# Kernel tuning notes

Hardware: AMD Instinct MI355X
Metric: run time of the kernel (lower is better)

Reference implementation:

```python
import jax, jax.numpy as jnp
import numpy as np

VOCAB, EMB = 30000, 300
HEADS, DPH = 8, 50
AD = HEADS * DPH            # att_dim_total = 400
MAX_LINES, MAX_WPL = 128, 32
BATCH = 16
NEG = 1e7                   # padding-mask penalty, matches torch source


def _split_heads(x):
    # [N, S, AD] -> [N, H, S, D]
    return x.reshape(x.shape[0], -1, HEADS, DPH).transpose(0, 2, 1, 3)


def _attention(q, k, v, mask_q=None, mask_k=None, mask_v=None):
    # Faithful port of MTHiSAN._attention. Note the (oddly named) torch masks:
    #   mask_q masks the KEY axis of scores, mask_k/mask_v zero the QUERY axis.
    scale = float(np.sqrt(q.shape[-1]))
    scores = jnp.einsum('bhqd,bhkd->bhqk', q, k) / scale
    if mask_q is not None:
        scores = scores - NEG * (~mask_q)[:, None, None, :].astype(scores.dtype)
    w = jax.nn.softmax(scores, axis=-1)
    if mask_k is not None:
        w = w * mask_k[:, None, :, None].astype(w.dtype)
    out = jnp.einsum('bhqk,bhkd->bhqd', w, v)
    if mask_v is not None:
        out = out * mask_v[:, None, :, None].astype(out.dtype)
    return out


def _forward(docs, emb, wq_w, wq_b, wk_w, wk_b, wv_w, wv_b, w_tgt,
             lq_w, lq_b, lk_w, lk_b, lv_w, lv_b, l_tgt,
             fc1_w, fc1_b, fc2_w, fc2_b):
    B = docs.shape[0]
    d = docs[:, :MAX_LINES * MAX_WPL].reshape(B * MAX_LINES, MAX_WPL)
    mask_w = d != 0                               # [B*L, W]
    mask_l = mask_w.sum(-1) != 0                  # [B*L]  non-empty lines
    # NOTE: instead of gathering non-empty lines (data-dependent shape), we keep
    # full shapes; masked word attention yields exact zeros for empty lines,
    # equivalent to the torch scatter into new_zeros.
    we = emb[d]                                   # [B*L, W, E] (dropout = eval/no-op)
    wq = jax.nn.elu(_split_heads(we @ wq_w + wq_b))
    wk = jax.nn.elu(_split_heads(we @ wk_w + wk_b))
    wv = jax.nn.elu(_split_heads(we @ wv_w + wv_b))
    watt = _attention(wq, wk, wv, mask_w, mask_w, mask_w)   # [B*L,H,W,D]
    # learned word-level target query (Linear(1, AD)(ones) == weight vector)
    tgt = jnp.broadcast_to(w_tgt.reshape(1, HEADS, 1, DPH),
                           (B * MAX_LINES, HEADS, 1, DPH))
    line_e = _attention(tgt, wk, watt, mask_q=mask_w)       # [B*L,H,1,D]
    line_e = line_e.transpose(0, 2, 1, 3).reshape(B * MAX_LINES, AD)
    line_e = line_e * mask_l[:, None].astype(line_e.dtype)  # zero empty lines
    line_e = line_e.reshape(B, MAX_LINES, AD)
    mask_l2 = mask_l.reshape(B, MAX_LINES)
    lq = jax.nn.elu(_split_heads(line_e @ lq_w + lq_b))
    lk = jax.nn.elu(_split_heads(line_e @ lk_w + lk_b))
    lv = jax.nn.elu(_split_heads(line_e @ lv_w + lv_b))
    latt = _attention(lq, lk, lv, mask_l2, mask_l2, mask_l2)  # [B,H,L,D]
    dtgt = jnp.broadcast_to(l_tgt.reshape(1, HEADS, 1, DPH), (B, HEADS, 1, DPH))
    doc_e = _attention(dtgt, lk, latt, mask_q=mask_l2)        # [B,H,1,D]
    doc_e = doc_e.transpose(0, 2, 1, 3).reshape(B, AD)
    logits1 = doc_e @ fc1_w + fc1_b   # task 'site'      [B,70]
    logits2 = doc_e @ fc2_w + fc2_b   # task 'histology' [B,512]
    return jnp.concatenate([logits1, logits2], axis=1)


def setup_inputs() -> dict:
    key = jax.random.key(0)
    ks = jax.random.split(key, 20)
    xavier = lambda k, i, o: (jax.random.normal(k, (i, o), jnp.float32)
                              * np.float32(np.sqrt(2.0 / (i + o))))
    emb = jax.random.normal(ks[0], (VOCAB, EMB), jnp.float32) * 0.02
    emb = emb.at[0].set(0.0)  # padding row zeroed as in __init__
    docs = jax.random.randint(ks[1], (BATCH, MAX_LINES * MAX_WPL), 0, VOCAB)
    z = lambda n: jnp.zeros((n,), jnp.float32)
    return dict(
        docs=docs, emb=emb,
        wq_w=xavier(ks[2], EMB, AD), wq_b=z(AD),
        wk_w=xavier(ks[3], EMB, AD), wk_b=z(AD),
        wv_w=xavier(ks[4], EMB, AD), wv_b=z(AD),
        w_tgt=jax.random.uniform(ks[5], (AD,), jnp.float32),
        lq_w=xavier(ks[6], AD, AD), lq_b=z(AD),
        lk_w=xavier(ks[7], AD, AD), lk_b=z(AD),
        lv_w=xavier(ks[8], AD, AD), lv_b=z(AD),
        l_tgt=jax.random.uniform(ks[9], (AD,), jnp.float32),
        fc1_w=xavier(ks[10], AD, 70), fc1_b=z(70),
        fc2_w=xavier(ks[11], AD, 512), fc2_b=z(512),
    )


def reference(docs, emb, wq_w, wq_b, wk_w, wk_b, wv_w, wv_b, w_tgt,
              lq_w, lq_b, lk_w, lk_b, lv_w, lv_b, l_tgt,
              fc1_w, fc1_b, fc2_w, fc2_b):
    return _forward(docs, emb, wq_w, wq_b, wk_w, wk_b, wv_w, wv_b, w_tgt,
                    lq_w, lq_b, lk_w, lk_b, lv_w, lv_b, l_tgt,
                    fc1_w, fc1_b, fc2_w, fc2_b)
```

## Files before the change

kernel.cpp:

```cpp
#include <hip/hip_runtime.h>
#include <math.h>

#define NLINES 2048
#define WPL 32
#define EMBD 300
#define AD 400
#define NH 8
#define DPH 50
#define QKV_S 52
#define SC_S 36
#define BATCH 16
#define LPD 128
#define NCOLS 1200
#define NPAD 1280
#define WLINE_FL 39936
#define HBLK 4992

typedef __bf16 bf16;
typedef bf16  v8bf  __attribute__((ext_vector_type(8)));
typedef float v4f   __attribute__((ext_vector_type(4)));
typedef float v16f  __attribute__((ext_vector_type(16)));

__device__ __forceinline__ float elu(float x) {
    return x > 0.f ? x : expm1f(x);
}
__device__ __forceinline__ float elu_fast(float x) {
    return x > 0.f ? x : (__expf(x) - 1.f);
}

#define SCALE 7.0710678118654755f

__global__ void split_rows(const float* __restrict__ src,
                           bf16* __restrict__ hi, bf16* __restrict__ lo,
                           int rows, int K, int K2)
{
    long idx = (long)blockIdx.x * 256 + threadIdx.x;
    if (idx >= (long)rows * K2) return;
    int r = (int)(idx / K2), k = (int)(idx - (long)r * K2);
    float x = (k < K) ? src[(long)r * K + k] : 0.f;
    bf16 h = (bf16)x;
    float hf = (float)h;
    bf16 l = (bf16)(x - hf);
    hi[idx] = h; lo[idx] = l;
}

__global__ void split_wt(const float* __restrict__ W0, const float* __restrict__ W1,
                         const float* __restrict__ W2,
                         const float* __restrict__ B0, const float* __restrict__ B1,
                         const float* __restrict__ B2,
                         bf16* __restrict__ hi, bf16* __restrict__ lo,
                         float* __restrict__ biasCat, int K, int K2)
{
    long idx = (long)blockIdx.x * 256 + threadIdx.x;
    if (idx >= (long)NPAD * K2) return;
    int n = (int)(idx / K2), k = (int)(idx - (long)n * K2);
    float x = 0.f;
    if (k < K && n < NCOLS) {
        int p = n / 400, c = n - p * 400;
        const float* W = (p == 0) ? W0 : (p == 1) ? W1 : W2;
        x = W[(long)k * 400 + c];
    }
    bf16 h = (bf16)x;
    float hf = (float)h;
    bf16 l = (bf16)(x - hf);
    hi[idx] = h; lo[idx] = l;
    if (k == 0) {
        float b = 0.f;
        if (n < NCOLS) {
            int p = n / 400, c = n - p * 400;
            const float* Bp = (p == 0) ? B0 : (p == 1) ? B1 : B2;
            b = Bp[c];
        }
        biasCat[n] = b;
    }
}

__launch_bounds__(256)
__global__ void mfma_gemm(const bf16* __restrict__ Ah_t, const bf16* __restrict__ Al_t,
                          const int* __restrict__ docs,
                          const bf16* __restrict__ Bh_t, const bf16* __restrict__ Bl_t,
                          const float* __restrict__ biasCat,
                          float* __restrict__ C, int K2, int word_layout)
{
    __shared__ __align__(16) bf16 Ah[4096];
    __shared__ __align__(16) bf16 Al[4096];
    __shared__ __align__(16) bf16 Bh[4096];
    __shared__ __align__(16) bf16 Bl[4096];
    __shared__ int tok[128];

    const int tid = threadIdx.x;
    const int row0 = blockIdx.y * 128;
    const int n0 = blockIdx.x * 128;

    if (tid < 128) tok[tid] = docs ? docs[row0 + tid] : (row0 + tid);
    __syncthreads();

    const int qa = tid >> 7;
    const int sm = tid & 127;
    const long aoff = (long)tok[sm] * K2;
    const long boff = (long)(n0 + sm) * K2;

    const int wv = tid >> 6, lane = tid & 63;
    const int half = lane >> 5, r32 = lane & 31;
    const int wm0 = (wv >> 1) * 64, wn0 = (wv & 1) * 64;

    v16f acc[2][2];
    #pragma unroll
    for (int a = 0; a < 2; ++a)
        #pragma unroll
        for (int b = 0; b < 2; ++b) acc[a][b] = (v16f)0.f;

    const int nk = K2 >> 5;
    v8bf pa0 = *(const v8bf*)(Ah_t + aoff + qa * 8);
    v8bf pa1 = *(const v8bf*)(Ah_t + aoff + (qa + 2) * 8);
    v8bf pl0 = *(const v8bf*)(Al_t + aoff + qa * 8);
    v8bf pl1 = *(const v8bf*)(Al_t + aoff + (qa + 2) * 8);
    v8bf pb0 = *(const v8bf*)(Bh_t + boff + qa * 8);
    v8bf pb1 = *(const v8bf*)(Bh_t + boff + (qa + 2) * 8);
    v8bf pc0 = *(const v8bf*)(Bl_t + boff + qa * 8);
    v8bf pc1 = *(const v8bf*)(Bl_t + boff + (qa + 2) * 8);

    for (int kt = 0; kt < nk; ++kt) {
        *(v8bf*)&Ah[tid * 8]         = pa0;
        *(v8bf*)&Ah[(256 + tid) * 8] = pa1;
        *(v8bf*)&Al[tid * 8]         = pl0;
        *(v8bf*)&Al[(256 + tid) * 8] = pl1;
        *(v8bf*)&Bh[tid * 8]         = pb0;
        *(v8bf*)&Bh[(256 + tid) * 8] = pb1;
        *(v8bf*)&Bl[tid * 8]         = pc0;
        *(v8bf*)&Bl[(256 + tid) * 8] = pc1;
        __syncthreads();

        if (kt + 1 < nk) {
            const int k1 = (kt + 1) * 32;
            pa0 = *(const v8bf*)(Ah_t + aoff + k1 + qa * 8);
            pa1 = *(const v8bf*)(Ah_t + aoff + k1 + (qa + 2) * 8);
            pl0 = *(const v8bf*)(Al_t + aoff + k1 + qa * 8);
            pl1 = *(const v8bf*)(Al_t + aoff + k1 + (qa + 2) * 8);
            pb0 = *(const v8bf*)(Bh_t + boff + k1 + qa * 8);
            pb1 = *(const v8bf*)(Bh_t + boff + k1 + (qa + 2) * 8);
            pc0 = *(const v8bf*)(Bl_t + boff + k1 + qa * 8);
            pc1 = *(const v8bf*)(Bl_t + boff + k1 + (qa + 2) * 8);
        }

        v8bf fa_h[2][2], fa_l[2][2], fb_h[2][2], fb_l[2][2];
        #pragma unroll
        for (int t = 0; t < 2; ++t)
            #pragma unroll
            for (int ks = 0; ks < 2; ++ks) {
                const int ea = (((ks * 2 + half) << 7) + wm0 + t * 32 + r32) * 8;
                fa_h[t][ks] = *(const v8bf*)&Ah[ea];
                fa_l[t][ks] = *(const v8bf*)&Al[ea];
                const int eb = (((ks * 2 + half) << 7) + wn0 + t * 32 + r32) * 8;
                fb_h[t][ks] = *(const v8bf*)&Bh[eb];
                fb_l[t][ks] = *(const v8bf*)&Bl[eb];
            }

        #pragma unroll
        for (int ks = 0; ks < 2; ++ks)
            #pragma unroll
            for (int mt = 0; mt < 2; ++mt)
                #pragma unroll
                for (int nt = 0; nt < 2; ++nt)
                    acc[mt][nt] = __builtin_amdgcn_mfma_f32_32x32x16_bf16(fa_h[mt][ks], fb_h[nt][ks], acc[mt][nt], 0, 0, 0);
        #pragma unroll
        for (int ks = 0; ks < 2; ++ks)
            #pragma unroll
            for (int mt = 0; mt < 2; ++mt)
                #pragma unroll
                for (int nt = 0; nt < 2; ++nt)
                    acc[mt][nt] = __builtin_amdgcn_mfma_f32_32x32x16_bf16(fa_h[mt][ks], fb_l[nt][ks], acc[mt][nt], 0, 0, 0);
        #pragma unroll
        for (int ks = 0; ks < 2; ++ks)
            #pragma unroll
            for (int mt = 0; mt < 2; ++mt)
                #pragma unroll
                for (int nt = 0; nt < 2; ++nt)
                    acc[mt][nt] = __builtin_amdgcn_mfma_f32_32x32x16_bf16(fa_l[mt][ks], fb_h[nt][ks], acc[mt][nt], 0, 0, 0);
        __syncthreads();
    }

    if (word_layout) {
        #pragma unroll
        for (int nt = 0; nt < 2; ++nt) {
            const int col = n0 + wn0 + nt * 32 + r32;
            if (col >= NCOLS) continue;
            const float bv = biasCat[col];
            const int p = col / 400;
            const int rem = col - p * 400;
            const int hh = rem / 50;
            const int d  = rem - hh * 50;
            #pragma unroll
            for (int mt = 0; mt < 2; ++mt) {
                const int rbase = row0 + wm0 + mt * 32 + 4 * half;
                #pragma unroll
                for (int rg = 0; rg < 16; ++rg) {
                    const int row = rbase + (rg & 3) + 8 * (rg >> 2);
                    const int ln = row >> 5, r = row & 31;
                    const float x = acc[mt][nt][rg] + bv;
                    C[(((long)ln * NH + hh) * 3 + p) * 1664 + r * 52 + d] = elu_fast(x);
                }
            }
        }
    } else {
        #pragma unroll
        for (int nt = 0; nt < 2; ++nt) {
            const int col = n0 + wn0 + nt * 32 + r32;
            if (col >= NCOLS) continue;
            const float bv = biasCat[col];
            #pragma unroll
            for (int mt = 0; mt < 2; ++mt) {
                const int rbase = row0 + wm0 + mt * 32 + 4 * half;
                #pragma unroll
                for (int rg = 0; rg < 16; ++rg) {
                    const int row = rbase + (rg & 3) + 8 * (rg >> 2);
                    const float x = acc[mt][nt][rg] + bv;
                    C[(long)row * NCOLS + col] = elu_fast(x);
                }
            }
        }
    }
}

__launch_bounds__(256)
__global__ void word_attn4(const float* __restrict__ qkvw, const int* __restrict__ docs,
                           const float* __restrict__ w_tgt,
                           float* __restrict__ line_e, float* __restrict__ mask_l)
{
    __shared__ __align__(16) float sh[HBLK];
    __shared__ float sc[32 * 33];
    __shared__ float msk[WPL];
    __shared__ float tw[WPL];
    __shared__ float coefA[WPL];
    __shared__ float part[8][33];
    __shared__ float cw[WPL];
    __shared__ float vpart[4][64];
    __shared__ float tg[52];
    __shared__ float mls_s;

    const int tid = threadIdx.x;
    const int line = blockIdx.x >> 3;
    const int h = blockIdx.x & 7;

    if (tid < WPL) msk[tid] = (docs[line * WPL + tid] != 0) ? 1.f : 0.f;
    if (tid >= 64 && tid < 116) tg[tid - 64] = (tid - 64 < DPH) ? w_tgt[h * DPH + tid - 64] : 0.f;

    const float* src = qkvw + ((long)line * NH + h) * HBLK;
    for (int i = tid; i < HBLK / 4; i += 256)
        *(float4*)&sh[i * 4] = *(const float4*)&src[i * 4];
    if (tid < 192) {
        const int a = tid / 64, rem = tid - a * 64;
        sh[a * 1664 + (rem >> 1) * 52 + 50 + (rem & 1)] = 0.f;
    }
    __syncthreads();

    if (tid == 0) {
        float m = 0.f;
        for (int w = 0; w < WPL; ++w) m = fmaxf(m, msk[w]);
        mls_s = m;
        if (h == 0) mask_l[line] = m;
    }

    const int j = tid >> 3, kg = tid & 7;
    float4 qv[13];
    #pragma unroll
    for (int i = 0; i < 13; ++i) qv[i] = *(const float4*)&sh[j * 52 + i * 4];

    float e4[4];
    float m = -1e30f;
    #pragma unroll
    for (int c = 0; c < 4; ++c) {
        const int kk = kg * 4 + c;
        const float* kr = &sh[1664 + kk * 52];
        float s = 0.f;
        #pragma unroll
        for (int i = 0; i < 13; ++i) {
            const float4 kv = *(const float4*)&kr[i * 4];
            s += qv[i].x * kv.x + qv[i].y * kv.y + qv[i].z * kv.z + qv[i].w * kv.w;
        }
        s = s / SCALE - 1e7f * (1.f - msk[kk]);
        e4[c] = s;
        m = fmaxf(m, s);
    }
    m = fmaxf(m, __shfl_xor(m, 1));
    m = fmaxf(m, __shfl_xor(m, 2));
    m = fmaxf(m, __shfl_xor(m, 4));
    float rsum = 0.f;
    #pragma unroll
    for (int c = 0; c < 4; ++c) { e4[c] = __expf(e4[c] - m); rsum += e4[c]; }
    rsum += __shfl_xor(rsum, 1);
    rsum += __shfl_xor(rsum, 2);
    rsum += __shfl_xor(rsum, 4);
    #pragma unroll
    for (int c = 0; c < 4; ++c) sc[j * 33 + kg * 4 + c] = e4[c];

    if (tid < WPL) {
        const float* kr = &sh[1664 + tid * 52];
        float s = 0.f;
        #pragma unroll
        for (int i = 0; i < 25; ++i)
            s += tg[2 * i] * kr[2 * i] + tg[2 * i + 1] * kr[2 * i + 1];
        s = s / SCALE - 1e7f * (1.f - msk[tid]);
        float tm = s;
        #pragma unroll
        for (int off = 16; off >= 1; off >>= 1) tm = fmaxf(tm, __shfl_xor(tm, off, 32));
        const float te = __expf(s - tm);
        float tsum = te;
        #pragma unroll
        for (int off = 16; off >= 1; off >>= 1) tsum += __shfl_xor(tsum, off, 32);
        tw[tid] = te / tsum;
    }
    __syncthreads();

    if (kg == 0) coefA[j] = tw[j] * msk[j] / rsum;
    __syncthreads();

    {
        const int k = tid & 31, jg = tid >> 5;
        float cv = 0.f;
        #pragma unroll
        for (int t = 0; t < 4; ++t) {
            const int jj = jg * 4 + t;
            cv += coefA[jj] * sc[jj * 33 + k];
        }
        part[jg][k] = cv;
    }
    __syncthreads();
    if (tid < WPL) {
        float cv = 0.f;
        #pragma unroll
        for (int g = 0; g < 8; ++g) cv += part[g][tid];
        cw[tid] = cv;
    }
    __syncthreads();

    {
        const int d = tid & 63, kh = tid >> 6;
        float acc = 0.f;
        if (d < 52) {
            #pragma unroll
            for (int t = 0; t < 8; ++t) {
                const int k = kh * 8 + t;
                acc += cw[k] * sh[3328 + k * 52 + d];
            }
        }
        vpart[kh][d] = acc;
    }
    __syncthreads();
    if (tid < DPH) {
        const float o = vpart[0][tid] + vpart[1][tid] + vpart[2][tid] + vpart[3][tid];
        line_e[(long)line * AD + h * DPH + tid] = o * mls_s;
    }
}

__launch_bounds__(256)
__global__ void line_attn2(const float* __restrict__ Q, const float* __restrict__ Kp,
                           const float* __restrict__ Vp,
                           long DS, long HS, long LS,
                           const float* __restrict__ l_tgt, const float* __restrict__ mask_l,
                           float* __restrict__ doc_e)
{
    __shared__ float kl[LPD * 52];
    __shared__ float sc[64 * 130];
    __shared__ float ml[LPD];
    __shared__ float tw[LPD];
    __shared__ float cw[LPD];
    __shared__ float coefA[64];
    __shared__ float pm[4 * 64];
    __shared__ float ps[4 * 64];
    __shared__ float tg[52];
    __shared__ float rr[2];
    __shared__ float vpart[2][64];

    const int tid = threadIdx.x;
    const int doc = blockIdx.x >> 3;
    const int h = blockIdx.x & 7;
    const float* qbase = Q + doc * DS + h * HS;
    const float* kbase = Kp + doc * DS + h * HS;
    const float* vbase = Vp + doc * DS + h * HS;

    if (tid < LPD) { ml[tid] = mask_l[doc * LPD + tid]; cw[tid] = 0.f; }
    if (tid < 52) tg[tid] = (tid < DPH) ? l_tgt[h * DPH + tid] : 0.f;
    for (int idx = tid; idx < LPD * 52; idx += 256) {
        const int r = idx / 52, d = idx - r * 52;
        kl[idx] = (d < DPH) ? kbase[(long)r * LS + d] : 0.f;
    }
    __syncthreads();

    if (tid < LPD) {
        const float* kr = &kl[tid * 52];
        float s = 0.f;
        #pragma unroll
        for (int i = 0; i < 25; ++i)
            s += tg[2 * i] * kr[2 * i] + tg[2 * i + 1] * kr[2 * i + 1];
        tw[tid] = s / SCALE - 1e7f * (1.f - ml[tid]);
    }
    __syncthreads();
    if (tid < 64) {
        float a = fmaxf(tw[tid], tw[64 + tid]);
        #pragma unroll
        for (int off = 32; off >= 1; off >>= 1) a = fmaxf(a, __shfl_xor(a, off));
        if (tid == 0) rr[0] = a;
    }
    __syncthreads();
    if (tid < 64) {
        const float tm2 = rr[0];
        float a = __expf(tw[tid] - tm2) + __expf(tw[64 + tid] - tm2);
        #pragma unroll
        for (int off = 32; off >= 1; off >>= 1) a += __shfl_xor(a, off);
        if (tid == 0) rr[1] = a;
    }
    __syncthreads();
    if (tid < LPD) tw[tid] = __expf(tw[tid] - rr[0]) / rr[1];
    __syncthreads();

    const int j2 = tid & 63;
    const int kq = tid >> 6;

    for (int g = 0; g < 2; ++g) {
        const int j = g * 64 + j2;
        float2 qv[25];
        #pragma unroll
        for (int i = 0; i < 25; ++i)
            qv[i] = *(const float2*)(qbase + (long)j * LS + 2 * i);

        float m = -1e30f;
        for (int c = 0; c < 32; ++c) {
            const int k = kq * 32 + c;
            const float* kr = &kl[k * 52];
            float s = 0.f;
            #pragma unroll
            for (int i = 0; i < 25; ++i)
                s += qv[i].x * kr[2 * i] + qv[i].y * kr[2 * i + 1];
            s = s / SCALE - 1e7f * (1.f - ml[k]);
            sc[j2 * 130 + k] = s;
            m = fmaxf(m, s);
        }
        pm[kq * 64 + j2] = m;
        __syncthreads();
        const float rowm = fmaxf(fmaxf(pm[j2], pm[64 + j2]),
                                 fmaxf(pm[128 + j2], pm[192 + j2]));
        float sum = 0.f;
        for (int c = 0; c < 32; ++c) {
            const int k = kq * 32 + c;
            const float e = __expf(sc[j2 * 130 + k] - rowm);
            sc[j2 * 130 + k] = e;
            sum += e;
        }
        ps[kq * 64 + j2] = sum;
        __syncthreads();
        if (kq == 0) {
            const float rs = ps[j2] + ps[64 + j2] + ps[128 + j2] + ps[192 + j2];
            coefA[j2] = tw[j] * ml[j] / rs;
        }
        __syncthreads();
        if (tid < LPD) {
            float cv = 0.f;
            for (int jj = 0; jj < 64; ++jj)
                cv += coefA[jj] * sc[jj * 130 + tid];
            cw[tid] += cv;
        }
        __syncthreads();
    }

    const int d = tid & 63;
    const int half = (tid >> 6) & 1;
    if (tid < 128 && d < DPH) {
        float acc = 0.f;
        for (int k = half * 64; k < half * 64 + 64; ++k)
            acc += cw[k] * vbase[(long)k * LS + d];
        vpart[half][d] = acc;
    }
    __syncthreads();
    if (tid < DPH)
        doc_e[doc * AD + h * DPH + tid] = vpart[0][tid] + vpart[1][tid];
}

__launch_bounds__(256)
__global__ void word_attn(const float* __restrict__ qkv, const int* __restrict__ docs,
                          const float* __restrict__ w_tgt,
                          float* __restrict__ line_e, float* __restrict__ mask_l)
{
    __shared__ float qs[WPL * QKV_S];
    __shared__ float ks[WPL * QKV_S];
    __shared__ float vs[WPL * QKV_S];
    __shared__ float sc[WPL * SC_S];
    __shared__ float ts[WPL], tw[WPL], cw[WPL], msk[WPL];
    __shared__ float mls;

    const int tid = threadIdx.x;
    const int line = blockIdx.x;

    if (tid < WPL) msk[tid] = (docs[line * WPL + tid] != 0) ? 1.f : 0.f;
    __syncthreads();
    if (tid == 0) {
        float ml = 0.f;
        for (int w = 0; w < WPL; ++w) ml = fmaxf(ml, msk[w]);
        mls = ml;
        mask_l[line] = ml;
    }
    for (int h = 0; h < NH; ++h) {
        for (int idx = tid; idx < WPL * DPH; idx += 256) {
            const int r = idx / DPH, d = idx - r * DPH;
            const size_t base = (size_t)(line * WPL + r) * NCOLS + h * DPH + d;
            qs[r * QKV_S + d] = qkv[base];
            ks[r * QKV_S + d] = qkv[base + 400];
            vs[r * QKV_S + d] = qkv[base + 800];
        }
        __syncthreads();
        {
            const int j = tid >> 3, kg = tid & 7;
            #pragma unroll
            for (int c = 0; c < 4; ++c) {
                const int kk = kg * 4 + c;
                float s = 0.f;
                for (int dd = 0; dd < DPH; ++dd)
                    s += qs[j * QKV_S + dd] * ks[kk * QKV_S + dd];
                sc[j * SC_S + kk] = s / SCALE - 1e7f * (1.f - msk[kk]);
            }
        }
        if (tid < WPL) {
            float s = 0.f;
            for (int dd = 0; dd < DPH; ++dd)
                s += w_tgt[h * DPH + dd] * ks[tid * QKV_S + dd];
            ts[tid] = s / SCALE - 1e7f * (1.f - msk[tid]);
        }
        __syncthreads();
        if (tid < WPL) {
            const int j = tid;
            float m = -1e30f;
            for (int kk = 0; kk < WPL; ++kk) m = fmaxf(m, sc[j * SC_S + kk]);
            float sum = 0.f;
            for (int kk = 0; kk < WPL; ++kk) {
                const float e = expf(sc[j * SC_S + kk] - m);
                sc[j * SC_S + kk] = e;
                sum += e;
            }
            const float inv = 1.f / sum;
            for (int kk = 0; kk < WPL; ++kk) sc[j * SC_S + kk] *= inv;
        } else if (tid == WPL) {
            float m = -1e30f;
            for (int jj = 0; jj < WPL; ++jj) m = fmaxf(m, ts[jj]);
            float sum = 0.f;
            for (int jj = 0; jj < WPL; ++jj) { const float e = expf(ts[jj] - m); tw[jj] = e; sum += e; }
            const float inv = 1.f / sum;
            for (int jj = 0; jj < WPL; ++jj) tw[jj] *= inv;
        }
        __syncthreads();
        if (tid < WPL) {
            const int kk = tid;
            float c = 0.f;
            for (int jj = 0; jj < WPL; ++jj) c += tw[jj] * msk[jj] * sc[jj * SC_S + kk];
            cw[kk] = c;
        }
        __syncthreads();
        if (tid < DPH) {
            float acc = 0.f;
            for (int kk = 0; kk < WPL; ++kk) acc += cw[kk] * vs[kk * QKV_S + tid];
            line_e[line * AD + h * DPH + tid] = acc * mls;
        }
        __syncthreads();
    }
}

__launch_bounds__(256, 2)
__global__ void gemm_qkv(const float* __restrict__ Asrc,
                         const int* __restrict__ docs,
                         const float* __restrict__ emb,
                         const float* __restrict__ W0, const float* __restrict__ W1,
                         const float* __restrict__ W2,
                         const float* __restrict__ B0, const float* __restrict__ B1,
                         const float* __restrict__ B2,
                         float* __restrict__ C, int M, int K)
{
    __shared__ __align__(16) float As[32][132];
    __shared__ __align__(16) float Bs[32][132];

    const int tid = threadIdx.x;
    const int row0 = blockIdx.x * 128;
    const int n0 = blockIdx.y * 128;
    const int tc = tid & 15, tr = tid >> 4;

    float acc[2][2][4][4];
    #pragma unroll
    for (int a = 0; a < 2; ++a)
        #pragma unroll
        for (int b = 0; b < 2; ++b)
            #pragma unroll
            for (int c = 0; c < 4; ++c)
                #pragma unroll
                for (int d = 0; d < 4; ++d) acc[a][b][c][d] = 0.f;

    const int ma = tid & 127;
    const int kq = tid >> 7;
    const float* arow;
    if (docs) arow = emb + (size_t)docs[row0 + ma] * EMBD;
    else      arow = Asrc + (size_t)(row0 + ma) * K;

    const int gcol = n0 + ma;
    const int p = gcol / 400;
    const int ccol = gcol - p * 400;
    const float* Wp = (p == 0) ? W0 : (p == 1) ? W1 : W2;
    const bool colv = gcol < NCOLS;

    const int nk = (K + 31) >> 5;
    for (int ck = 0; ck < nk; ++ck) {
        const int k0 = ck * 32;
        #pragma unroll
        for (int f = 0; f < 4; ++f) {
            const int kl = kq * 16 + f * 4;
            const int kg = k0 + kl;
            float4 v = make_float4(0.f, 0.f, 0.f, 0.f);
            if (kg < K) v = *(const float4*)(arow + kg);
            As[kl + 0][ma] = v.x;
            As[kl + 1][ma] = v.y;
            As[kl + 2][ma] = v.z;
            As[kl + 3][ma] = v.w;
        }
        #pragma unroll
        for (int i = 0; i < 16; ++i) {
            const int kl = kq * 16 + i;
            const int kg = k0 + kl;
            float v = 0.f;
            if (colv && kg < K) v = Wp[(size_t)kg * 400 + ccol];
            Bs[kl][ma] = v;
        }
        __syncthreads();

        #pragma unroll 8
        for (int k = 0; k < 32; ++k) {
            const float4 a0 = *(const float4*)&As[k][tr * 4];
            const float4 a1 = *(const float4*)&As[k][64 + tr * 4];
            const float4 b0 = *(const float4*)&Bs[k][tc * 4];
            const float4 b1 = *(const float4*)&Bs[k][64 + tc * 4];
            const float ar[2][4] = {{a0.x, a0.y, a0.z, a0.w}, {a1.x, a1.y, a1.z, a1.w}};
            const float br[2][4] = {{b0.x, b0.y, b0.z, b0.w}, {b1.x, b1.y, b1.z, b1.w}};
            #pragma unroll
            for (int im = 0; im < 2; ++im)
                #pragma unroll
                for (int in_ = 0; in_ < 2; ++in_)
                    #pragma unroll
                    for (int rr = 0; rr < 4; ++rr)
                        #pragma unroll
                        for (int cc = 0; cc < 4; ++cc)
                            acc[im][in_][rr][cc] += ar[im][rr] * br[in_][cc];
        }
        __syncthreads();
    }

    #pragma unroll
    for (int in_ = 0; in_ < 2; ++in_) {
        const int ncol = n0 + in_ * 64 + tc * 4;
        if (ncol >= NCOLS) continue;
        const int pj = ncol / 400;
        const int cj = ncol - pj * 400;
        const float* Bp = (pj == 0) ? B0 : (pj == 1) ? B1 : B2;
        const float4 bv = *(const float4*)(Bp + cj);
        #pragma unroll
        for (int im = 0; im < 2; ++im) {
            #pragma unroll
            for (int rr = 0; rr < 4; ++rr) {
                const int row = row0 + im * 64 + tr * 4 + rr;
                float4 o;
                o.x = elu(acc[im][in_][rr][0] + bv.x);
                o.y = elu(acc[im][in_][rr][1] + bv.y);
                o.z = elu(acc[im][in_][rr][2] + bv.z);
                o.w = elu(acc[im][in_][rr][3] + bv.w);
                *(float4*)(C + (size_t)row * NCOLS + ncol) = o;
            }
        }
    }
}

__global__ void logits_kernel(const float* __restrict__ doc_e,
                              const float* __restrict__ fc1_w, const float* __restrict__ fc1_b,
                              const float* __restrict__ fc2_w, const float* __restrict__ fc2_b,
                              float* __restrict__ out)
{
    int o = blockIdx.x * blockDim.x + threadIdx.x;
    if (o >= BATCH * 582) return;
    int b = o / 582, jj = o - b * 582;
    const float* de = doc_e + b * AD;
    float acc;
    if (jj < 70) {
        acc = fc1_b[jj];
        for (int k = 0; k < AD; ++k) acc += de[k] * fc1_w[k * 70 + jj];
    } else {
        int j2 = jj - 70;
        acc = fc2_b[j2];
        for (int k = 0; k < AD; ++k) acc += de[k] * fc2_w[k * 512 + j2];
    }
    out[o] = acc;
}

extern "C" void kernel_launch(void* const* d_in, const int* in_sizes, int n_in,
                              void* d_out, int out_size, void* d_ws, size_t ws_size,
                              hipStream_t stream) {
    const int*   docs  = (const int*)  d_in[0];
    const float* emb   = (const float*)d_in[1];
    const float* wq_w  = (const float*)d_in[2];
    const float* wq_b  = (const float*)d_in[3];
    const float* wk_w  = (const float*)d_in[4];
    const float* wk_b  = (const float*)d_in[5];
    const float* wv_w  = (const float*)d_in[6];
    const float* wv_b  = (const float*)d_in[7];
    const float* w_tgt = (const float*)d_in[8];
    const float* lq_w  = (const float*)d_in[9];
    const float* lq_b  = (const float*)d_in[10];
    const float* lk_w  = (const float*)d_in[11];
    const float* lk_b  = (const float*)d_in[12];
    const float* lv_w  = (const float*)d_in[13];
    const float* lv_b  = (const float*)d_in[14];
    const float* l_tgt = (const float*)d_in[15];
    const float* fc1_w = (const float*)d_in[16];
    const float* fc1_b = (const float*)d_in[17];
    const float* fc2_w = (const float*)d_in[18];
    const float* fc2_b = (const float*)d_in[19];
    float* out = (float*)d_out;
    float* ws = (float*)d_ws;

    const long O_LINE_E = 0;
    const long O_MASK_L = 819200;
    const long O_DOC_E  = 821248;
    const long O_BIAS_W = 827648;
    const long O_BIAS_L = 828928;
    const long O_EMB_H  = 830208;
    const long O_EMB_L  = 5630208;
    const long O_WTW_H  = 10430208;
    const long O_WTW_L  = 10635008;
    const long O_WTL_H  = 10839808;
    const long O_WTL_L  = 11106048;
    const long O_LE_H   = 11372288;
    const long O_LE_L   = 11798272;
    const long O_R      = 12224256;

    const long LINE_QKV_FL = (long)NLINES * NCOLS;
    long ws_fl = (long)(ws_size / 4);
    long Rcap = ws_fl - O_R;

    if (Rcap >= LINE_QKV_FL) {
        float* line_e = ws + O_LINE_E;
        float* mask_l = ws + O_MASK_L;
        float* doc_e  = ws + O_DOC_E;
        float* bias_w = ws + O_BIAS_W;
        float* bias_l = ws + O_BIAS_L;
        bf16* embh = (bf16*)(ws + O_EMB_H);
        bf16* embl = (bf16*)(ws + O_EMB_L);
        bf16* wtwh = (bf16*)(ws + O_WTW_H);
        bf16* wtwl = (bf16*)(ws + O_WTW_L);
        bf16* wtlh = (bf16*)(ws + O_WTL_H);
        bf16* wtll = (bf16*)(ws + O_WTL_L);
        bf16* leh  = (bf16*)(ws + O_LE_H);
        bf16* lel  = (bf16*)(ws + O_LE_L);
        float* R   = ws + O_R;

        split_rows<<<(30000L * 320 + 255) / 256, 256, 0, stream>>>(emb, embh, embl, 30000, 300, 320);
        split_wt<<<((long)NPAD * 320 + 255) / 256, 256, 0, stream>>>(wq_w, wk_w, wv_w,
                                                                     wq_b, wk_b, wv_b,
                                                                     wtwh, wtwl, bias_w, 300, 320);
        split_wt<<<((long)NPAD * 416 + 255) / 256, 256, 0, stream>>>(lq_w, lk_w, lv_w,
                                                                     lq_b, lk_b, lv_b,
                                                                     wtlh, wtll, bias_l, 400, 416);

        long maxl = Rcap / WLINE_FL;
        if (maxl > 1024) maxl = 1024;
        long chunk = (maxl / 4) * 4;
        if (chunk < 4) chunk = 4;
        for (long c0 = 0; c0 < NLINES; c0 += chunk) {
            long cl = NLINES - c0 < chunk ? NLINES - c0 : chunk;
            dim3 g1(10, (unsigned)((cl * 32) / 128));
            mfma_gemm<<<g1, 256, 0, stream>>>(embh, embl, docs + c0 * WPL,
                                              wtwh, wtwl, bias_w, R, 320, 1);
            word_attn4<<<(unsigned)(cl * NH), 256, 0, stream>>>(R, docs + c0 * WPL, w_tgt,
                                                                line_e + c0 * AD, mask_l + c0);
        }

        split_rows<<<((long)NLINES * 416 + 255) / 256, 256, 0, stream>>>(line_e, leh, lel,
                                                                         NLINES, 400, 416);
        dim3 g2(10, NLINES / 128);
        mfma_gemm<<<g2, 256, 0, stream>>>(leh, lel, nullptr, wtlh, wtll, bias_l, R, 416, 0);
        line_attn2<<<BATCH * NH, 256, 0, stream>>>(R, R + 400, R + 800,
                                                   (long)LPD * NCOLS, (long)DPH, (long)NCOLS,
                                                   l_tgt, mask_l, doc_e);
        logits_kernel<<<(BATCH * 582 + 255) / 256, 256, 0, stream>>>(doc_e, fc1_w, fc1_b,
                                                                     fc2_w, fc2_b, out);
    } else {
        const long F_FIXED = 827648;
        const long PER_LINE_FL = (long)WPL * NCOLS;
        float* line_e = ws;
        float* mask_l = ws + 819200;
        float* doc_e  = ws + 821248;
        float* R      = ws + F_FIXED;
        long Rcap2 = ws_fl - F_FIXED;

        long maxl = Rcap2 / PER_LINE_FL;
        if (maxl > NLINES) maxl = NLINES;
        long maxl4 = (maxl / 4) * 4;
        int nc = (int)((NLINES + maxl4 - 1) / maxl4);
        int chunk = (int)((NLINES + nc - 1) / nc);
        chunk = ((chunk + 3) / 4) * 4;

        for (int c0 = 0; c0 < NLINES; c0 += chunk) {
            int cl = NLINES - c0 < chunk ? NLINES - c0 : chunk;
            dim3 g1((cl * 32) / 128, 10);
            gemm_qkv<<<g1, 256, 0, stream>>>(nullptr, docs + (size_t)c0 * WPL, emb,
                                             wq_w, wk_w, wv_w, wq_b, wk_b, wv_b,
                                             R, cl * 32, EMBD);
            word_attn<<<cl, 256, 0, stream>>>(R, docs + (size_t)c0 * WPL, w_tgt,
                                              line_e + (size_t)c0 * AD, mask_l + c0);
        }
        dim3 g2(16, 10);
        gemm_qkv<<<g2, 256, 0, stream>>>(line_e, nullptr, emb,
                                         lq_w, lk_w, lv_w, lq_b, lk_b, lv_b,
                                         R, NLINES, AD);
        line_attn2<<<BATCH * NH, 256, 0, stream>>>(R, R + 400, R + 800,
                                                   (long)LPD * NCOLS, (long)DPH, (long)NCOLS,
                                                   l_tgt, mask_l, doc_e);
        logits_kernel<<<(BATCH * 582 + 255) / 256, 256, 0, stream>>>(doc_e, fc1_w, fc1_b,
                                                                     fc2_w, fc2_b, out);
    }
}
```

Measured before the change: 655.5 us.

## Double-buffer GEMM tiles via direct global-to-LDS loads and swizzle block order

Replaces the register-staged global loads in the split-bf16 MFMA GEMM with global_load_lds direct-to-LDS copies into a double-buffered shared array, so the next K tile loads while the current one is computed and one barrier per iteration is dropped. It also remaps the flat block index so consecutive blocks are spread across groups of eight, for better cache locality. The word-layout epilogue now writes the two padding zeros per row, which lets the attention kernel drop its LDS zeroing. The costs are doubled LDS use, which may reduce occupancy, and reliance on the LDS-DMA load path.

```diff
diff --git a/kernel.cpp b/kernel.cpp
--- a/kernel.cpp
+++ b/kernel.cpp
@@ -29,6 +29,13 @@
 }
 
 #define SCALE 7.0710678118654755f
+
+__device__ __forceinline__ void gld16(const bf16* g, bf16* l) {
+    __builtin_amdgcn_global_load_lds(
+        (const __attribute__((address_space(1))) void*)(g),
+        (__attribute__((address_space(3))) void*)(l),
+        16, 0, 0);
+}
 
 __global__ void split_rows(const float* __restrict__ src,
                            bf16* __restrict__ hi, bf16* __restrict__ lo,
@@ -82,23 +89,26 @@
                           const float* __restrict__ biasCat,
                           float* __restrict__ C, int K2, int word_layout)
 {
-    __shared__ __align__(16) bf16 Ah[4096];
-    __shared__ __align__(16) bf16 Al[4096];
-    __shared__ __align__(16) bf16 Bh[4096];
-    __shared__ __align__(16) bf16 Bl[4096];
+    __shared__ __align__(16) bf16 lds[2][4][4096];
     __shared__ int tok[128];
 
     const int tid = threadIdx.x;
-    const int row0 = blockIdx.y * 128;
-    const int n0 = blockIdx.x * 128;
+
+    const int total = (int)(gridDim.x * gridDim.y);
+    int flat = (int)(blockIdx.y * gridDim.x + blockIdx.x);
+    if ((total & 7) == 0) flat = (flat & 7) * (total >> 3) + (flat >> 3);
+    const int bx = flat % (int)gridDim.x;
+    const int by = flat / (int)gridDim.x;
+    const int row0 = by * 128;
+    const int n0 = bx * 128;
 
     if (tid < 128) tok[tid] = docs ? docs[row0 + tid] : (row0 + tid);
     __syncthreads();
 
-    const int qa = tid >> 7;
-    const int sm = tid & 127;
-    const long aoff = (long)tok[sm] * K2;
-    const long boff = (long)(n0 + sm) * K2;
+    const int qa0 = tid >> 7;
+    const long abase = (long)tok[tid & 127] * K2;
+    const long bbase = (long)(n0 + (tid & 127)) * K2;
+    const int wb = tid & ~63;
 
     const int wv = tid >> 6, lane = tid & 63;
     const int half = lane >> 5, r32 = lane & 31;
@@ -110,50 +120,44 @@
         #pragma unroll
         for (int b = 0; b < 2; ++b) acc[a][b] = (v16f)0.f;
 
+    auto STAGE = [&](int buf, int k0) {
+        const bf16* ga = Ah_t + abase + k0;
+        const bf16* gl = Al_t + abase + k0;
+        const bf16* gb = Bh_t + bbase + k0;
+        const bf16* gc = Bl_t + bbase + k0;
+        bf16* L0 = &lds[buf][0][wb * 8];
+        bf16* L1 = &lds[buf][1][wb * 8];
+        bf16* L2 = &lds[buf][2][wb * 8];
+        bf16* L3 = &lds[buf][3][wb * 8];
+        gld16(ga + qa0 * 8,       L0);
+        gld16(ga + (qa0 + 2) * 8, L0 + 2048);
+        gld16(gl + qa0 * 8,       L1);
+        gld16(gl + (qa0 + 2) * 8, L1 + 2048);
+        gld16(gb + qa0 * 8,       L2);
+        gld16(gb + (qa0 + 2) * 8, L2 + 2048);
+        gld16(gc + qa0 * 8,       L3);
+        gld16(gc + (qa0 + 2) * 8, L3 + 2048);
+    };
+
     const int nk = K2 >> 5;
-    v8bf pa0 = *(const v8bf*)(Ah_t + aoff + qa * 8);
-    v8bf pa1 = *(const v8bf*)(Ah_t + aoff + (qa + 2) * 8);
-    v8bf pl0 = *(const v8bf*)(Al_t + aoff + qa * 8);
-    v8bf pl1 = *(const v8bf*)(Al_t + aoff + (qa + 2) * 8);
-    v8bf pb0 = *(const v8bf*)(Bh_t + boff + qa * 8);
-    v8bf pb1 = *(const v8bf*)(Bh_t + boff + (qa + 2) * 8);
-    v8bf pc0 = *(const v8bf*)(Bl_t + boff + qa * 8);
-    v8bf pc1 = *(const v8bf*)(Bl_t + boff + (qa + 2) * 8);
-
+    STAGE(0, 0);
+    __syncthreads();
+
+    int cur = 0;
     for (int kt = 0; kt < nk; ++kt) {
-        *(v8bf*)&Ah[tid * 8]         = pa0;
-        *(v8bf*)&Ah[(256 + tid) * 8] = pa1;
-        *(v8bf*)&Al[tid * 8]         = pl0;
-        *(v8bf*)&Al[(256 + tid) * 8] = pl1;
-        *(v8bf*)&Bh[tid * 8]         = pb0;
-        *(v8bf*)&Bh[(256 + tid) * 8] = pb1;
-        *(v8bf*)&Bl[tid * 8]         = pc0;
-        *(v8bf*)&Bl[(256 + tid) * 8] = pc1;
-        __syncthreads();
-
-        if (kt + 1 < nk) {
-            const int k1 = (kt + 1) * 32;
-            pa0 = *(const v8bf*)(Ah_t + aoff + k1 + qa * 8);
-            pa1 = *(const v8bf*)(Ah_t + aoff + k1 + (qa + 2) * 8);
-            pl0 = *(const v8bf*)(Al_t + aoff + k1 + qa * 8);
-            pl1 = *(const v8bf*)(Al_t + aoff + k1 + (qa + 2) * 8);
-            pb0 = *(const v8bf*)(Bh_t + boff + k1 + qa * 8);
-            pb1 = *(const v8bf*)(Bh_t + boff + k1 + (qa + 2) * 8);
-            pc0 = *(const v8bf*)(Bl_t + boff + k1 + qa * 8);
-            pc1 = *(const v8bf*)(Bl_t + boff + k1 + (qa + 2) * 8);
-        }
+        if (kt + 1 < nk) STAGE(cur ^ 1, (kt + 1) * 32);
 
         v8bf fa_h[2][2], fa_l[2][2], fb_h[2][2], fb_l[2][2];
         #pragma unroll
         for (int t = 0; t < 2; ++t)
             #pragma unroll
             for (int ks = 0; ks < 2; ++ks) {
-                const int ea = (((ks * 2 + half) << 7) + wm0 + t * 32 + r32) * 8;
-                fa_h[t][ks] = *(const v8bf*)&Ah[ea];
-                fa_l[t][ks] = *(const v8bf*)&Al[ea];
+                const int e = (((ks * 2 + half) << 7) + wm0 + t * 32 + r32) * 8;
+                fa_h[t][ks] = *(const v8bf*)&lds[cur][0][e];
+                fa_l[t][ks] = *(const v8bf*)&lds[cur][1][e];
                 const int eb = (((ks * 2 + half) << 7) + wn0 + t * 32 + r32) * 8;
-                fb_h[t][ks] = *(const v8bf*)&Bh[eb];
-                fb_l[t][ks] = *(const v8bf*)&Bl[eb];
+                fb_h[t][ks] = *(const v8bf*)&lds[cur][2][eb];
+                fb_l[t][ks] = *(const v8bf*)&lds[cur][3][eb];
             }
 
         #pragma unroll
@@ -177,7 +181,9 @@
                 #pragma unroll
                 for (int nt = 0; nt < 2; ++nt)
                     acc[mt][nt] = __builtin_amdgcn_mfma_f32_32x32x16_bf16(fa_l[mt][ks], fb_h[nt][ks], acc[mt][nt], 0, 0, 0);
-        __syncthreads();
+
+        __syncthreads();
+        cur ^= 1;
     }
 
     if (word_layout) {
@@ -197,8 +203,13 @@
                 for (int rg = 0; rg < 16; ++rg) {
                     const int row = rbase + (rg & 3) + 8 * (rg >> 2);
                     const int ln = row >> 5, r = row & 31;
+                    const long base = (((long)ln * NH + hh) * 3 + p) * 1664 + r * 52;
                     const float x = acc[mt][nt][rg] + bv;
-                    C[(((long)ln * NH + hh) * 3 + p) * 1664 + r * 52 + d] = elu_fast(x);
+                    C[base + d] = elu_fast(x);
+                    if (d == 49) {
+                        float2 z; z.x = 0.f; z.y = 0.f;
+                        *(float2*)&C[base + 50] = z;
+                    }
                 }
             }
         }
@@ -248,10 +259,6 @@
     const float* src = qkvw + ((long)line * NH + h) * HBLK;
     for (int i = tid; i < HBLK / 4; i += 256)
         *(float4*)&sh[i * 4] = *(const float4*)&src[i * 4];
-    if (tid < 192) {
-        const int a = tid / 64, rem = tid - a * 64;
-        sh[a * 1664 + (rem >> 1) * 52 + 50 + (rem & 1)] = 0.f;
-    }
     __syncthreads();
 
     if (tid == 0) {
```

Measured after the change: 640.0 us. 2.4% less time.
